# Optimization experiments

Measured on AMD Instinct MI355X. Metric: run time of the kernel, lower is better.

## Reference

```python
import jax, jax.numpy as jnp
import numpy as np

B, T, N, F_, H, C, E = 8, 16, 1024, 128, 8, 32, 32768
D = H * C  # 256 = hidden_channels * num_heads
NEG_SLOPE = 0.2


def setup_inputs() -> dict:
    key = jax.random.key(0)
    ks = jax.random.split(key, 16)
    p = lambda k, shape: (jax.random.normal(k, shape, jnp.float32) * 0.05)
    inp = {
        "x": jax.random.normal(ks[0], (B, T, N, F_), jnp.float32),
        "edge_index": jax.random.randint(ks[1], (2, E), 0, N, jnp.int64),
        "edge_weight": jax.random.uniform(ks[2], (E,), jnp.float32),
        # GAT layer 1
        "W1": p(ks[3], (F_, D)), "att_src1": p(ks[4], (H, C)),
        "att_dst1": p(ks[5], (H, C)), "b1": jnp.zeros((D,), jnp.float32),
        # GAT layer 2
        "W2": p(ks[6], (D, D)), "att_src2": p(ks[7], (H, C)),
        "att_dst2": p(ks[8], (H, C)), "b2": jnp.zeros((D,), jnp.float32),
        # LSTM (torch gate order: i, f, g, o)
        "lstm_Wih": p(ks[9], (4 * D, D)), "lstm_Whh": p(ks[10], (4 * D, D)),
        "lstm_bih": jnp.zeros((4 * D,), jnp.float32),
        "lstm_bhh": jnp.zeros((4 * D,), jnp.float32),
        # edge predictors
        "Wp": p(ks[11], (1, D)), "bp": jnp.zeros((1,), jnp.float32),
        "Wc": p(ks[12], (1, D)), "bc": jnp.zeros((1,), jnp.float32),
    }
    return inp


def _gat_layer(x2d, src, dst, W, a_src, a_dst, b):
    # x2d: [N, Fin]; src/dst: [Et] (self-loops already appended)
    h = (x2d @ W).reshape(N, H, C)              # [N, H, C]
    es = jnp.sum(h * a_src, axis=-1)            # [N, H]
    ed = jnp.sum(h * a_dst, axis=-1)            # [N, H]
    e = jax.nn.leaky_relu(es[src] + ed[dst], NEG_SLOPE)  # [Et, H]
    m = jax.ops.segment_max(e, dst, num_segments=N)      # [N, H]
    m = jnp.where(jnp.isfinite(m), m, 0.0)
    pnum = jnp.exp(e - m[dst])                  # [Et, H]
    denom = jax.ops.segment_sum(pnum, dst, num_segments=N)
    alpha = pnum / (denom[dst] + 1e-16)         # segment softmax over incoming edges
    out = jax.ops.segment_sum(alpha[:, :, None] * h[src], dst, num_segments=N)
    return out.reshape(N, D) + b                # concat heads + bias


def _forward(x, edge_index, edge_weight, W1, att_src1, att_dst1, b1,
             W2, att_src2, att_dst2, b2, lstm_Wih, lstm_Whh, lstm_bih,
             lstm_bhh, Wp, bp, Wc, bc):
    # GATConv ignores edge_weight when edge_dim is None (lin_edge is None).
    sl = jnp.arange(N, dtype=edge_index.dtype)
    src = jnp.concatenate([edge_index[0], sl])  # add_self_loops=True
    dst = jnp.concatenate([edge_index[1], sl])

    def per_graph(xi):  # xi: [N, F_]
        hh = jax.nn.relu(_gat_layer(xi, src, dst, W1, att_src1, att_dst1, b1))
        hh = jax.nn.relu(_gat_layer(hh, src, dst, W2, att_src2, att_dst2, b2))
        return hh  # [N, D]

    # stack timesteps then batches == reshape to [B*T, N, F_]
    hall = jax.vmap(per_graph)(x.reshape(B * T, N, F_))  # [B*T, N, D]

    # LSTM over the node dimension (batch_first=True, batch=B*T, seq=N)
    def step(carry, xt):
        hprev, cprev = carry
        z = xt @ lstm_Wih.T + hprev @ lstm_Whh.T + lstm_bih + lstm_bhh
        i, f, g, o = jnp.split(z, 4, axis=-1)
        c = jax.nn.sigmoid(f) * cprev + jax.nn.sigmoid(i) * jnp.tanh(g)
        hcur = jax.nn.sigmoid(o) * jnp.tanh(c)
        return (hcur, hcur * 0 + c)[0:1] * 0 or ((hcur, c), hcur)

    def step2(carry, xt):
        hprev, cprev = carry
        z = xt @ lstm_Wih.T + hprev @ lstm_Whh.T + lstm_bih + lstm_bhh
        i, f, g, o = jnp.split(z, 4, axis=-1)
        c = jax.nn.sigmoid(f) * cprev + jax.nn.sigmoid(i) * jnp.tanh(g)
        hcur = jax.nn.sigmoid(o) * jnp.tanh(c)
        return (hcur, c), hcur

    init = (jnp.zeros((B * T, D), hall.dtype), jnp.zeros((B * T, D), hall.dtype))
    _, hs = jax.lax.scan(step2, init, jnp.swapaxes(hall, 0, 1))  # [N, B*T, D]
    out = jnp.swapaxes(hs, 0, 1)      # [B*T, N, D]

    xsel = out[::T]                   # [B, N, D]
    xflat = xsel.reshape(B * N, D)
    xe = xflat[edge_index[0]] * xflat[edge_index[1]]  # [E, D]
    edge_weights_pred = xe @ Wp.T + bp                # [E, 1]
    logits = (xe @ Wc.T + bc).squeeze(-1)             # [E]
    return edge_weights_pred, logits


def reference(x, edge_index, edge_weight, W1, att_src1, att_dst1, b1,
              W2, att_src2, att_dst2, b2, lstm_Wih, lstm_Whh, lstm_bih,
              lstm_bhh, Wp, bp, Wc, bc):
    return _forward(x, edge_index, edge_weight, W1, att_src1, att_dst1, b1,
                    W2, att_src2, att_dst2, b2, lstm_Wih, lstm_Whh, lstm_bih,
                    lstm_bhh, Wp, bp, Wc, bc)
```

## Files before the change

### kernel.cpp

```cpp
#include <hip/hip_runtime.h>
#include <math.h>

#define NN 1024
#define FF 128
#define DD 256
#define HH 8
#define CC 32
#define EE 32768
#define NEDGE (EE + NN)

typedef unsigned int u32x4 __attribute__((ext_vector_type(4)));

__device__ __forceinline__ float sigf(float x) { return 1.0f / (1.0f + expf(-x)); }
__device__ __forceinline__ float fsig(float x) { return 1.0f / (1.0f + __expf(-x)); }
__device__ __forceinline__ float ftanh(float x) { return 2.0f / (1.0f + __expf(-2.0f * x)) - 1.0f; }

__device__ __forceinline__ void store_l2_u64(unsigned long long* p, unsigned long long v) {
  asm volatile("global_store_dwordx2 %0, %1, off sc0" :: "v"(p), "v"(v) : "memory");
}
__device__ __forceinline__ u32x4 load_l2_x4(const unsigned long long* p) {
  u32x4 r;
  asm volatile("global_load_dwordx4 %0, %1, off sc0\n\ts_waitcnt vmcnt(0)"
               : "=v"(r) : "v"(p) : "memory");
  return r;
}

__global__ void k_count(const int* __restrict__ ei, int* __restrict__ count) {
  int k = blockIdx.x * blockDim.x + threadIdx.x;
  if (k >= NEDGE) return;
  int d = (k < EE) ? ei[EE + k] : (k - EE);
  atomicAdd(&count[d], 1);
}

__global__ void k_scan(const int* __restrict__ count, int* __restrict__ rowptr, int* __restrict__ cursor) {
  __shared__ int buf[NN];
  int t = threadIdx.x;
  int c = count[t];
  buf[t] = c;
  __syncthreads();
  for (int off = 1; off < NN; off <<= 1) {
    int add = (t >= off) ? buf[t - off] : 0;
    __syncthreads();
    buf[t] += add;
    __syncthreads();
  }
  int inc = buf[t];
  rowptr[t] = inc - c;
  cursor[t] = inc - c;
  if (t == NN - 1) rowptr[NN] = inc;
}

__global__ void k_scatter(const int* __restrict__ ei, int* __restrict__ cursor, int* __restrict__ csrc) {
  int k = blockIdx.x * blockDim.x + threadIdx.x;
  if (k >= NEDGE) return;
  int s, d;
  if (k < EE) { s = ei[k]; d = ei[EE + k]; }
  else        { s = k - EE; d = k - EE; }
  int pos = atomicAdd(&cursor[d], 1);
  csrc[pos] = s;
}

template<bool BT, bool ADDB>
__global__ __launch_bounds__(256) void k_gemm(const float* __restrict__ A, const float* __restrict__ B,
    const float* __restrict__ bias1, const float* __restrict__ bias2, float* __restrict__ C,
    int M, int N, int K) {
  __shared__ float At[64][17];
  __shared__ float Bt[16][65];
  const int tid = threadIdx.x;
  const int m0 = blockIdx.x * 64, n0 = blockIdx.y * 64;
  const int tx = tid & 15, ty = tid >> 4;
  float acc[4][4] = {{0.f, 0.f, 0.f, 0.f}};
  for (int k0 = 0; k0 < K; k0 += 16) {
    {
      int rr = tid >> 2, kl = (tid & 3) * 4;
      float4 a = *(const float4*)(A + (m0 + rr) * K + k0 + kl);
      At[rr][kl] = a.x; At[rr][kl + 1] = a.y; At[rr][kl + 2] = a.z; At[rr][kl + 3] = a.w;
    }
    if (BT) {
      int nn = tid >> 2, kl = (tid & 3) * 4;
      float4 b = *(const float4*)(B + (n0 + nn) * K + k0 + kl);
      Bt[kl][nn] = b.x; Bt[kl + 1][nn] = b.y; Bt[kl + 2][nn] = b.z; Bt[kl + 3][nn] = b.w;
    } else {
      int kk = tid >> 4, nn = (tid & 15) * 4;
      float4 b = *(const float4*)(B + (k0 + kk) * N + n0 + nn);
      Bt[kk][nn] = b.x; Bt[kk][nn + 1] = b.y; Bt[kk][nn + 2] = b.z; Bt[kk][nn + 3] = b.w;
    }
    __syncthreads();
    #pragma unroll
    for (int kk = 0; kk < 16; ++kk) {
      float av[4], bv[4];
      #pragma unroll
      for (int i = 0; i < 4; ++i) av[i] = At[ty * 4 + i][kk];
      #pragma unroll
      for (int jj = 0; jj < 4; ++jj) bv[jj] = Bt[kk][tx * 4 + jj];
      #pragma unroll
      for (int i = 0; i < 4; ++i)
        #pragma unroll
        for (int jj = 0; jj < 4; ++jj)
          acc[i][jj] = fmaf(av[i], bv[jj], acc[i][jj]);
    }
    __syncthreads();
  }
  #pragma unroll
  for (int i = 0; i < 4; ++i) {
    #pragma unroll
    for (int jj = 0; jj < 4; ++jj) {
      int n = n0 + tx * 4 + jj;
      float v = acc[i][jj];
      if (ADDB) v += bias1[n] + bias2[n];
      C[(m0 + ty * 4 + i) * N + n] = v;
    }
  }
}

__global__ __launch_bounds__(256) void k_att(const float* __restrict__ h, const float* __restrict__ asrc,
    const float* __restrict__ adst, float* __restrict__ es, float* __restrict__ ed) {
  int n = blockIdx.x;
  int hd = threadIdx.x >> 5, c = threadIdx.x & 31;
  float hv = h[n * DD + hd * CC + c];
  float e1 = hv * asrc[hd * CC + c];
  float e2 = hv * adst[hd * CC + c];
  #pragma unroll
  for (int msk = 1; msk < 32; msk <<= 1) { e1 += __shfl_xor(e1, msk); e2 += __shfl_xor(e2, msk); }
  if (c == 0) { es[n * HH + hd] = e1; ed[n * HH + hd] = e2; }
}

__global__ __launch_bounds__(256) void k_agg(const float* __restrict__ h, const float* __restrict__ es,
    const float* __restrict__ ed, const float* __restrict__ bias, const int* __restrict__ rowptr,
    const int* __restrict__ csrc, float* __restrict__ out) {
  int w = blockIdx.x * 4 + (threadIdx.x >> 6);
  int lane = threadIdx.x & 63;
  int n = w >> 3, hd = w & 7;
  int lo = rowptr[n], hi = rowptr[n + 1];
  float edn = ed[n * HH + hd];
  float m = -1e30f;
  for (int k = lo + lane; k < hi; k += 64) {
    int s = csrc[k];
    float e = es[s * HH + hd] + edn;
    e = (e > 0.f) ? e : 0.2f * e;
    m = fmaxf(m, e);
  }
  #pragma unroll
  for (int msk = 1; msk < 64; msk <<= 1) m = fmaxf(m, __shfl_xor(m, msk));
  float den = 0.f;
  for (int k = lo + lane; k < hi; k += 64) {
    int s = csrc[k];
    float e = es[s * HH + hd] + edn;
    e = (e > 0.f) ? e : 0.2f * e;
    den += expf(e - m);
  }
  #pragma unroll
  for (int msk = 1; msk < 64; msk <<= 1) den += __shfl_xor(den, msk);
  float inv = 1.0f / (den + 1e-16f);
  int c = lane & 31, halfsel = lane >> 5;
  float acc = 0.f;
  for (int k = lo + halfsel; k < hi; k += 2) {
    int s = csrc[k];
    float e = es[s * HH + hd] + edn;
    e = (e > 0.f) ? e : 0.2f * e;
    float al = expf(e - m) * inv;
    acc += al * h[s * DD + hd * CC + c];
  }
  acc += __shfl_down(acc, 32);
  if (lane < 32) {
    float v = acc + bias[hd * CC + c];
    out[n * DD + hd * CC + c] = fmaxf(v, 0.f);
  }
}

__global__ __launch_bounds__(256, 1) void k_lstm(const float* __restrict__ xW,
    const float* __restrict__ Whh, unsigned long long* __restrict__ fastw,
    unsigned long long* __restrict__ sloww, float* __restrict__ hs) {
  const int bid = blockIdx.x;
  const int coh = bid & 7;
  const int j = bid >> 3;
  unsigned long long* fw = fastw + coh * 2 * DD;
  unsigned long long* sw = sloww + coh * 2 * DD;
  const int t = threadIdx.x;
  const int r = t >> 1, half = t & 1;
  const int g = r >> 5, kl = r & 31;
  const int grow = g * 256 + j * 32 + kl;
  __shared__ float hlds[DD];
  __shared__ float zlds[128];

  float4 w[32];
  {
    const float4* W4 = (const float4*)(Whh + grow * DD + half * 128);
    #pragma unroll
    for (int q = 0; q < 32; ++q)
      asm volatile("global_load_dwordx4 %0, %1, off" : "=v"(w[q]) : "v"(W4 + q));
    asm volatile("s_waitcnt vmcnt(0)" ::: "memory");
  }
  if (t < DD) hlds[t] = 0.f;
  float creg = 0.f;
  float xwv = xW[grow];
  int ftries = 48, miss = 0;
  int bud = 1 << 24;
  __syncthreads();

  for (int s = 0; s < NN; ++s) {
    const float4* h4 = ((const float4*)hlds) + half * 32;
    float ac4[4] = {0.f, 0.f, 0.f, 0.f};
    #pragma unroll
    for (int q = 0; q < 32; ++q) {
      float4 hv = h4[q];
      ac4[q & 3] = fmaf(w[q].x, hv.x, ac4[q & 3]);
      ac4[q & 3] = fmaf(w[q].y, hv.y, ac4[q & 3]);
      ac4[q & 3] = fmaf(w[q].z, hv.z, ac4[q & 3]);
      ac4[q & 3] = fmaf(w[q].w, hv.w, ac4[q & 3]);
    }
    float acc = (ac4[0] + ac4[1]) + (ac4[2] + ac4[3]);
    acc += __shfl_xor(acc, 1);
    if (half == 0) zlds[r] = acc + xwv;
    __syncthreads();

    const int par = (s + 1) & 1;
    const unsigned int tag = (unsigned int)(s + 1);
    float xw_next = (s + 1 < NN) ? xW[(s + 1) * 1024 + grow] : 0.f;

    if (t < 32) {
      float iv = zlds[t], fv = zlds[32 + t], gv = zlds[64 + t], ov = zlds[96 + t];
      creg = fsig(fv) * creg + fsig(iv) * ftanh(gv);
      float hn = fsig(ov) * ftanh(creg);
      int col = j * 32 + t;
      hlds[col] = hn;
      unsigned long long pk = ((unsigned long long)__float_as_uint(hn) << 32) | tag;
      store_l2_u64(&fw[par * DD + col], pk);
      __hip_atomic_store(&sw[par * DD + col], pk, __ATOMIC_RELAXED, __HIP_MEMORY_SCOPE_AGENT);
      hs[s * DD + col] = hn;
    } else if (t >= 64 && t < 176) {
      int pi = t - 64;
      int peer = j + 1 + (pi >> 4); if (peer >= 8) peer -= 8;
      int col0 = peer * 32 + ((pi & 15) << 1);
      int idx = par * DD + col0;
      u32x4 v; bool got = false;
      for (int tr = 0; tr < ftries; ++tr) {
        v = load_l2_x4(&fw[idx]);
        if (v.x == tag && v.z == tag) { got = true; break; }
      }
      if (!got) {
        ++miss;
        unsigned long long a, b;
        for (;;) {
          a = __hip_atomic_load(&sw[idx], __ATOMIC_RELAXED, __HIP_MEMORY_SCOPE_AGENT);
          if ((unsigned int)(a & 0xffffffffULL) == tag) break;
          if (--bud <= 0) break;
          __builtin_amdgcn_s_sleep(1);
        }
        for (;;) {
          b = __hip_atomic_load(&sw[idx + 1], __ATOMIC_RELAXED, __HIP_MEMORY_SCOPE_AGENT);
          if ((unsigned int)(b & 0xffffffffULL) == tag) break;
          if (--bud <= 0) break;
          __builtin_amdgcn_s_sleep(1);
        }
        v.y = (unsigned int)(a >> 32);
        v.w = (unsigned int)(b >> 32);
        if (miss >= 2 && ftries > 2) ftries = 2;
      }
      hlds[col0] = __uint_as_float(v.y);
      hlds[col0 + 1] = __uint_as_float(v.w);
    }
    __syncthreads();
    xwv = xw_next;
  }
}

__global__ __launch_bounds__(256) void k_edges(const float* __restrict__ hs, const int* __restrict__ ei,
    const float* __restrict__ Wp, const float* __restrict__ bp,
    const float* __restrict__ Wc, const float* __restrict__ bc, float* __restrict__ out) {
  int widx = threadIdx.x >> 6, lane = threadIdx.x & 63;
  int k = blockIdx.x * 4 + widx;
  int sIdx = ei[k], dIdx = ei[EE + k];
  float4 u = ((const float4*)(hs + sIdx * DD))[lane];
  float4 v = ((const float4*)(hs + dIdx * DD))[lane];
  float4 wp = ((const float4*)Wp)[lane];
  float4 wc = ((const float4*)Wc)[lane];
  float x0 = u.x * v.x, x1 = u.y * v.y, x2 = u.z * v.z, x3 = u.w * v.w;
  float ap = x0 * wp.x + x1 * wp.y + x2 * wp.z + x3 * wp.w;
  float ac = x0 * wc.x + x1 * wc.y + x2 * wc.z + x3 * wc.w;
  #pragma unroll
  for (int msk = 1; msk < 64; msk <<= 1) { ap += __shfl_xor(ap, msk); ac += __shfl_xor(ac, msk); }
  if (lane == 0) { out[k] = ap + bp[0]; out[EE + k] = ac + bc[0]; }
}

extern "C" void kernel_launch(void* const* d_in, const int* in_sizes, int n_in,
                              void* d_out, int out_size, void* d_ws, size_t ws_size,
                              hipStream_t stream) {
  const float* x       = (const float*)d_in[0];
  const int* ei        = (const int*)d_in[1];
  const float* W1      = (const float*)d_in[3];
  const float* as1     = (const float*)d_in[4];
  const float* ad1     = (const float*)d_in[5];
  const float* b1      = (const float*)d_in[6];
  const float* W2      = (const float*)d_in[7];
  const float* as2     = (const float*)d_in[8];
  const float* ad2     = (const float*)d_in[9];
  const float* b2      = (const float*)d_in[10];
  const float* Wih     = (const float*)d_in[11];
  const float* Whh     = (const float*)d_in[12];
  const float* bih     = (const float*)d_in[13];
  const float* bhh     = (const float*)d_in[14];
  const float* Wp      = (const float*)d_in[15];
  const float* bp      = (const float*)d_in[16];
  const float* Wc      = (const float*)d_in[17];
  const float* bc      = (const float*)d_in[18];
  float* out = (float*)d_out;

  char* ws = (char*)d_ws;
  int* counts                = (int*)(ws + 0);
  unsigned long long* fastw  = (unsigned long long*)(ws + 4096);
  unsigned long long* sloww  = (unsigned long long*)(ws + 36864);
  int* rowptr                = (int*)(ws + 69632);
  int* cursor                = (int*)(ws + 77824);
  int* csrc                  = (int*)(ws + 81920);
  float* es                  = (float*)(ws + 221184);
  float* ed                  = (float*)(ws + 253952);
  float* buf0                = (float*)(ws + 286720);
  float* buf1                = (float*)(ws + 1335296);
  float* xW                  = (float*)(ws + 2383872);
  float* hsall               = (float*)(ws + 6578176);

  hipMemsetAsync(ws, 0, 69632, stream);

  k_count  <<<(NEDGE + 255) / 256, 256, 0, stream>>>(ei, counts);
  k_scan   <<<1, 1024, 0, stream>>>(counts, rowptr, cursor);
  k_scatter<<<(NEDGE + 255) / 256, 256, 0, stream>>>(ei, cursor, csrc);

  k_gemm<false, false><<<dim3(16, 4), 256, 0, stream>>>(x, W1, nullptr, nullptr, buf0, NN, DD, FF);
  k_att<<<NN, 256, 0, stream>>>(buf0, as1, ad1, es, ed);
  k_agg<<<NN * HH / 4, 256, 0, stream>>>(buf0, es, ed, b1, rowptr, csrc, buf1);

  k_gemm<false, false><<<dim3(16, 4), 256, 0, stream>>>(buf1, W2, nullptr, nullptr, buf0, NN, DD, DD);
  k_att<<<NN, 256, 0, stream>>>(buf0, as2, ad2, es, ed);
  k_agg<<<NN * HH / 4, 256, 0, stream>>>(buf0, es, ed, b2, rowptr, csrc, buf1);

  k_gemm<true, true><<<dim3(16, 16), 256, 0, stream>>>(buf1, Wih, bih, bhh, xW, NN, 1024, DD);

  k_lstm<<<64, 256, 0, stream>>>(xW, Whh, fastw, sloww, hsall);

  k_edges<<<EE / 4, 256, 0, stream>>>(hsall, ei, Wp, bp, Wc, bc, out);
}
```

Baseline: 1.976 ms.

## Split LSTM recurrent dot product across four threads per row with 512-thread blocks

The persistent LSTM kernel now uses 512 threads per block, with four threads per gate row each covering 64 weights, where before two threads per row each covered 128. This halves the per-thread serial FMA chain and register footprint at the cost of an extra shuffle reduction. Peer hidden-state exchange now uses one thread per column with 8-byte polls instead of one per column pair with 16-byte polls. The fast-poll fallback heuristic is also changed to count only misses after the first few steps.

```diff
diff --git a/kernel.cpp b/kernel.cpp
--- a/kernel.cpp
+++ b/kernel.cpp
@@ -9,7 +9,7 @@
 #define EE 32768
 #define NEDGE (EE + NN)
 
-typedef unsigned int u32x4 __attribute__((ext_vector_type(4)));
+typedef unsigned int u32x2 __attribute__((ext_vector_type(2)));
 
 __device__ __forceinline__ float sigf(float x) { return 1.0f / (1.0f + expf(-x)); }
 __device__ __forceinline__ float fsig(float x) { return 1.0f / (1.0f + __expf(-x)); }
@@ -18,9 +18,9 @@
 __device__ __forceinline__ void store_l2_u64(unsigned long long* p, unsigned long long v) {
   asm volatile("global_store_dwordx2 %0, %1, off sc0" :: "v"(p), "v"(v) : "memory");
 }
-__device__ __forceinline__ u32x4 load_l2_x4(const unsigned long long* p) {
-  u32x4 r;
-  asm volatile("global_load_dwordx4 %0, %1, off sc0\n\ts_waitcnt vmcnt(0)"
+__device__ __forceinline__ u32x2 load_l2_u64(const unsigned long long* p) {
+  u32x2 r;
+  asm volatile("global_load_dwordx2 %0, %1, off sc0\n\ts_waitcnt vmcnt(0)"
                : "=v"(r) : "v"(p) : "memory");
   return r;
 }
@@ -168,7 +168,7 @@
   }
 }
 
-__global__ __launch_bounds__(256, 1) void k_lstm(const float* __restrict__ xW,
+__global__ __launch_bounds__(512, 1) void k_lstm(const float* __restrict__ xW,
     const float* __restrict__ Whh, unsigned long long* __restrict__ fastw,
     unsigned long long* __restrict__ sloww, float* __restrict__ hs) {
   const int bid = blockIdx.x;
@@ -177,32 +177,32 @@
   unsigned long long* fw = fastw + coh * 2 * DD;
   unsigned long long* sw = sloww + coh * 2 * DD;
   const int t = threadIdx.x;
-  const int r = t >> 1, half = t & 1;
+  const int r = t >> 2, qt = t & 3;
   const int g = r >> 5, kl = r & 31;
   const int grow = g * 256 + j * 32 + kl;
   __shared__ float hlds[DD];
   __shared__ float zlds[128];
 
-  float4 w[32];
+  float4 w[16];
   {
-    const float4* W4 = (const float4*)(Whh + grow * DD + half * 128);
+    const float4* W4 = (const float4*)(Whh + grow * DD + qt * 64);
     #pragma unroll
-    for (int q = 0; q < 32; ++q)
+    for (int q = 0; q < 16; ++q)
       asm volatile("global_load_dwordx4 %0, %1, off" : "=v"(w[q]) : "v"(W4 + q));
     asm volatile("s_waitcnt vmcnt(0)" ::: "memory");
   }
   if (t < DD) hlds[t] = 0.f;
   float creg = 0.f;
   float xwv = xW[grow];
-  int ftries = 48, miss = 0;
+  int ftries = 64, lateMiss = 0;
   int bud = 1 << 24;
   __syncthreads();
 
   for (int s = 0; s < NN; ++s) {
-    const float4* h4 = ((const float4*)hlds) + half * 32;
+    const float4* h4 = ((const float4*)hlds) + qt * 16;
     float ac4[4] = {0.f, 0.f, 0.f, 0.f};
     #pragma unroll
-    for (int q = 0; q < 32; ++q) {
+    for (int q = 0; q < 16; ++q) {
       float4 hv = h4[q];
       ac4[q & 3] = fmaf(w[q].x, hv.x, ac4[q & 3]);
       ac4[q & 3] = fmaf(w[q].y, hv.y, ac4[q & 3]);
@@ -211,7 +211,8 @@
     }
     float acc = (ac4[0] + ac4[1]) + (ac4[2] + ac4[3]);
     acc += __shfl_xor(acc, 1);
-    if (half == 0) zlds[r] = acc + xwv;
+    acc += __shfl_xor(acc, 2);
+    if (qt == 0) zlds[r] = acc + xwv;
     __syncthreads();
 
     const int par = (s + 1) & 1;
@@ -228,37 +229,29 @@
       store_l2_u64(&fw[par * DD + col], pk);
       __hip_atomic_store(&sw[par * DD + col], pk, __ATOMIC_RELAXED, __HIP_MEMORY_SCOPE_AGENT);
       hs[s * DD + col] = hn;
-    } else if (t >= 64 && t < 176) {
+    } else if (t >= 64 && t < 288) {
       int pi = t - 64;
-      int peer = j + 1 + (pi >> 4); if (peer >= 8) peer -= 8;
-      int col0 = peer * 32 + ((pi & 15) << 1);
-      int idx = par * DD + col0;
-      u32x4 v; bool got = false;
+      int peer = j + 1 + (pi >> 5); if (peer >= 8) peer -= 8;
+      int col = peer * 32 + (pi & 31);
+      int idx = par * DD + col;
+      u32x2 v; bool got = false;
       for (int tr = 0; tr < ftries; ++tr) {
-        v = load_l2_x4(&fw[idx]);
-        if (v.x == tag && v.z == tag) { got = true; break; }
+        v = load_l2_u64(&fw[idx]);
+        if (v.x == tag) { got = true; break; }
       }
       if (!got) {
-        ++miss;
-        unsigned long long a, b;
+        if (s >= 4) ++lateMiss;
+        if (lateMiss >= 8 && ftries > 2) ftries = 2;
+        unsigned long long a;
         for (;;) {
           a = __hip_atomic_load(&sw[idx], __ATOMIC_RELAXED, __HIP_MEMORY_SCOPE_AGENT);
           if ((unsigned int)(a & 0xffffffffULL) == tag) break;
           if (--bud <= 0) break;
           __builtin_amdgcn_s_sleep(1);
         }
-        for (;;) {
-          b = __hip_atomic_load(&sw[idx + 1], __ATOMIC_RELAXED, __HIP_MEMORY_SCOPE_AGENT);
-          if ((unsigned int)(b & 0xffffffffULL) == tag) break;
-          if (--bud <= 0) break;
-          __builtin_amdgcn_s_sleep(1);
-        }
         v.y = (unsigned int)(a >> 32);
-        v.w = (unsigned int)(b >> 32);
-        if (miss >= 2 && ftries > 2) ftries = 2;
       }
-      hlds[col0] = __uint_as_float(v.y);
-      hlds[col0 + 1] = __uint_as_float(v.w);
+      hlds[col] = __uint_as_float(v.y);
     }
     __syncthreads();
     xwv = xw_next;
@@ -336,7 +329,7 @@
 
   k_gemm<true, true><<<dim3(16, 16), 256, 0, stream>>>(buf1, Wih, bih, bhh, xW, NN, 1024, DD);
 
-  k_lstm<<<64, 256, 0, stream>>>(xW, Whh, fastw, sloww, hsall);
+  k_lstm<<<64, 512, 0, stream>>>(xW, Whh, fastw, sloww, hsall);
 
   k_edges<<<EE / 4, 256, 0, stream>>>(hsall, ei, Wp, bp, Wc, bc, out);
 }
```

New measurement: 2.156 ms. 9.1% more time.
